# Kernel optimization log

Hardware: AMD Instinct MI355X
Metric: run time of the kernel (lower is better)

The kernel has to match this reference:

```python
import jax, jax.numpy as jnp
import numpy as np

VOCAB = 50000
D = 300
S = 5
CTX = 10
B = 16384

def setup_inputs() -> dict:
    key = jax.random.key(0)
    k1, k2, k3 = jax.random.split(key, 3)
    x = jax.random.randint(k1, (B, 2 + CTX), 0, VOCAB, dtype=jnp.int32)
    W_g = jax.random.normal(k2, (VOCAB, D), dtype=jnp.float32)
    W_s = jax.random.normal(k3, (VOCAB, S, D), dtype=jnp.float32)
    return {"x": x, "W_g": W_g, "W_s": W_s}

def reference(x, W_g, W_s):
    # sum of context word global vectors: gather (B, CTX, D) -> sum -> (B, D)
    sum_context = jnp.sum(W_g[x[:, 2:]], axis=1)
    # sense vectors of target word: (B, S, D)
    sense_vecs = W_s[x[:, 0]]
    # per-sense dot with context (theano scan over senses): (S, B)
    scores = jnp.einsum('bsd,bd->sb', sense_vecs, sum_context)
    # (right_senses / context_sense_vectors are dead code in the original)
    # literal translation: sigmoid of sum over axis=1 of (S, B) -> (S,)
    return jax.nn.sigmoid(jnp.sum(scores, axis=1))
```

## Files before the change

kernel.cpp:

```cpp
#include <hip/hip_runtime.h>

#define BATCH 16384
#define DDIM  300
#define NS    5
#define NCTX  10
#define XSTR  (NCTX + 2)
#define D4    75
#define NBLK  2048

__global__ __launch_bounds__(256) void sense_partials(
    const int*   __restrict__ x,
    const float* __restrict__ Wg,
    const float* __restrict__ Ws,
    float*       __restrict__ partial ) {
  const int lane = threadIdx.x & 63;
  const int wid  = threadIdx.x >> 6;
  const int gw   = blockIdx.x * 4 + wid;
  const int nw   = NBLK * 4;

  float acc[NS] = {0.f, 0.f, 0.f, 0.f, 0.f};

  for (int b = gw; b < BATCH; b += nw) {
    const int* xr = x + b * XSTR;
    int v = (lane < XSTR) ? xr[lane] : 0;
    const int w0 = __shfl(v, 0);

    float4 sc0 = make_float4(0.f, 0.f, 0.f, 0.f);
    float4 sc1 = make_float4(0.f, 0.f, 0.f, 0.f);
#pragma unroll
    for (int j = 0; j < NCTX; ++j) {
      const int c = __shfl(v, 2 + j);
      const float4* row = (const float4*)Wg + (size_t)c * D4;
      float4 r0 = row[lane];
      sc0.x += r0.x; sc0.y += r0.y; sc0.z += r0.z; sc0.w += r0.w;
      if (lane < D4 - 64) {
        float4 r1 = row[64 + lane];
        sc1.x += r1.x; sc1.y += r1.y; sc1.z += r1.z; sc1.w += r1.w;
      }
    }

    const float4* wrow = (const float4*)Ws + (size_t)w0 * (NS * D4);
#pragma unroll
    for (int s = 0; s < NS; ++s) {
      float4 a0 = wrow[s * D4 + lane];
      float d = a0.x * sc0.x + a0.y * sc0.y + a0.z * sc0.z + a0.w * sc0.w;
      if (lane < D4 - 64) {
        float4 a1 = wrow[s * D4 + 64 + lane];
        d += a1.x * sc1.x + a1.y * sc1.y + a1.z * sc1.z + a1.w * sc1.w;
      }
      acc[s] += d;
    }
  }

#pragma unroll
  for (int s = 0; s < NS; ++s) {
    float t = acc[s];
#pragma unroll
    for (int off = 32; off; off >>= 1) t += __shfl_down(t, off);
    acc[s] = t;
  }

  __shared__ float red[4][NS];
  if (lane == 0) {
#pragma unroll
    for (int s = 0; s < NS; ++s) red[wid][s] = acc[s];
  }
  __syncthreads();
  if (threadIdx.x < NS) {
    float t = red[0][threadIdx.x] + red[1][threadIdx.x] +
              red[2][threadIdx.x] + red[3][threadIdx.x];
    partial[threadIdx.x * NBLK + blockIdx.x] = t;
  }
}

__global__ __launch_bounds__(320) void sense_reduce(
    const float* __restrict__ partial, float* __restrict__ out) {
  const int lane = threadIdx.x & 63;
  const int s    = threadIdx.x >> 6;
  float sum = 0.f;
  for (int g = lane; g < NBLK; g += 64) sum += partial[s * NBLK + g];
#pragma unroll
  for (int off = 32; off; off >>= 1) sum += __shfl_down(sum, off);
  if (lane == 0) out[s] = 1.0f / (1.0f + __expf(-sum));
}

extern "C" void kernel_launch(void* const* d_in, const int* in_sizes, int n_in,
                              void* d_out, int out_size, void* d_ws, size_t ws_size,
                              hipStream_t stream) {
  const int*   x  = (const int*)d_in[0];
  const float* Wg = (const float*)d_in[1];
  const float* Ws = (const float*)d_in[2];
  float* partial  = (float*)d_ws;
  float* out      = (float*)d_out;

  sense_partials<<<NBLK, 256, 0, stream>>>(x, Wg, Ws, partial);
  sense_reduce<<<1, 320, 0, stream>>>(partial, out);
}
```

Before: 421.4 us.

## Process two batch rows per wave and use nontemporal loads for sense vectors

Replaces the grid-stride loop with a fixed mapping where each wave handles two batch rows. This doubles the independent gathers in flight per wave. The sense-vector reads from W_s now use nontemporal loads, so streamed data is less likely to evict W_g rows from cache. The mapping relies on NBLK*4*2 equaling BATCH exactly, and per-wave register use rises.

Result: faster. 405.7 us (-3.7%).

```diff
diff --git a/kernel.cpp b/kernel.cpp
--- a/kernel.cpp
+++ b/kernel.cpp
@@ -1,7 +1,8 @@
 #include <hip/hip_runtime.h>
 
+typedef float v4f __attribute__((ext_vector_type(4)));
+
 #define BATCH 16384
-#define DDIM  300
 #define NS    5
 #define NCTX  10
 #define XSTR  (NCTX + 2)
@@ -15,41 +16,48 @@
     float*       __restrict__ partial ) {
   const int lane = threadIdx.x & 63;
   const int wid  = threadIdx.x >> 6;
-  const int gw   = blockIdx.x * 4 + wid;
-  const int nw   = NBLK * 4;
+  const int pair = blockIdx.x * 4 + wid;
+  const int b0   = pair * 2;
 
-  float acc[NS] = {0.f, 0.f, 0.f, 0.f, 0.f};
+  const v4f* Wg4 = (const v4f*)Wg;
+  const v4f* Ws4 = (const v4f*)Ws;
 
-  for (int b = gw; b < BATCH; b += nw) {
-    const int* xr = x + b * XSTR;
-    int v = (lane < XSTR) ? xr[lane] : 0;
-    const int w0 = __shfl(v, 0);
+  int v = (lane < 2 * XSTR) ? x[(size_t)b0 * XSTR + lane] : 0;
+  const int wA = __shfl(v, 0);
+  const int wB = __shfl(v, XSTR);
 
-    float4 sc0 = make_float4(0.f, 0.f, 0.f, 0.f);
-    float4 sc1 = make_float4(0.f, 0.f, 0.f, 0.f);
+  const v4f* WsA = Ws4 + (size_t)wA * (NS * D4);
+  const v4f* WsB = Ws4 + (size_t)wB * (NS * D4);
+
+  const bool hi = (lane < D4 - 64);
+
+  v4f sA0 = 0.f, sA1 = 0.f, sB0 = 0.f, sB1 = 0.f;
 #pragma unroll
-    for (int j = 0; j < NCTX; ++j) {
-      const int c = __shfl(v, 2 + j);
-      const float4* row = (const float4*)Wg + (size_t)c * D4;
-      float4 r0 = row[lane];
-      sc0.x += r0.x; sc0.y += r0.y; sc0.z += r0.z; sc0.w += r0.w;
-      if (lane < D4 - 64) {
-        float4 r1 = row[64 + lane];
-        sc1.x += r1.x; sc1.y += r1.y; sc1.z += r1.z; sc1.w += r1.w;
-      }
+  for (int j = 0; j < NCTX; ++j) {
+    const int ca = __shfl(v, 2 + j);
+    const int cb = __shfl(v, XSTR + 2 + j);
+    const v4f* ra = Wg4 + (size_t)ca * D4;
+    const v4f* rb = Wg4 + (size_t)cb * D4;
+    sA0 += ra[lane];
+    sB0 += rb[lane];
+    if (hi) {
+      sA1 += ra[64 + lane];
+      sB1 += rb[64 + lane];
     }
+  }
 
-    const float4* wrow = (const float4*)Ws + (size_t)w0 * (NS * D4);
+  float acc[NS];
 #pragma unroll
-    for (int s = 0; s < NS; ++s) {
-      float4 a0 = wrow[s * D4 + lane];
-      float d = a0.x * sc0.x + a0.y * sc0.y + a0.z * sc0.z + a0.w * sc0.w;
-      if (lane < D4 - 64) {
-        float4 a1 = wrow[s * D4 + 64 + lane];
-        d += a1.x * sc1.x + a1.y * sc1.y + a1.z * sc1.z + a1.w * sc1.w;
-      }
-      acc[s] += d;
+  for (int s = 0; s < NS; ++s) {
+    v4f a0 = __builtin_nontemporal_load(&WsA[s * D4 + lane]);
+    v4f c0 = __builtin_nontemporal_load(&WsB[s * D4 + lane]);
+    v4f p  = a0 * sA0 + c0 * sB0;
+    if (hi) {
+      v4f a1 = __builtin_nontemporal_load(&WsA[s * D4 + 64 + lane]);
+      v4f c1 = __builtin_nontemporal_load(&WsB[s * D4 + 64 + lane]);
+      p += a1 * sA1 + c1 * sB1;
     }
+    acc[s] = p.x + p.y + p.z + p.w;
   }
 
 #pragma unroll
```
